# Performance work log

Measured on AMD Instinct MI355X. Metric: run time of the kernel, lower is better.

The kernel has to match this reference:

```python
import jax, jax.numpy as jnp
import numpy as np

N = 100_000          # nodes
E = 3_200_000        # edges (avg degree 32)
DIMS = [6, 20, 15, 10, 5, 2]


def setup_inputs() -> dict:
    key = jax.random.key(0)
    ks = jax.random.split(key, 3 + 2 * 5)
    inp = {
        "x": jax.random.normal(ks[0], (N, DIMS[0]), jnp.float32),
        "edge_index": jax.random.randint(ks[1], (2, E), 0, N, jnp.int32),
        "edge_weight": jax.random.uniform(ks[2], (E,), jnp.float32),
    }
    for i in range(5):
        din, dout = DIMS[i], DIMS[i + 1]
        s = 1.0 / np.sqrt(din)
        inp[f"w_rel{i}"] = jax.random.normal(ks[3 + 2 * i], (din, dout), jnp.float32) * s
        inp[f"b_rel{i}"] = jnp.zeros((dout,), jnp.float32)
        inp[f"w_root{i}"] = jax.random.normal(ks[4 + 2 * i], (din, dout), jnp.float32) * s
    return inp


def _graph_conv(x, src, dst, w, W_rel, b_rel, W_root):
    # PyG GraphConv: lin_rel(scatter_add(w_e * x_src)) + lin_root(x)
    msg = x[src] * w[:, None]                                  # [E, din]
    agg = jax.ops.segment_sum(msg, dst, num_segments=N)        # [N, din]
    return agg @ W_rel + b_rel + x @ W_root                    # [N, dout]


def reference(x, edge_index, edge_weight,
              w_rel0, b_rel0, w_root0,
              w_rel1, b_rel1, w_root1,
              w_rel2, b_rel2, w_root2,
              w_rel3, b_rel3, w_root3,
              w_rel4, b_rel4, w_root4):
    src, dst = edge_index[0], edge_index[1]
    layers = [
        (w_rel0, b_rel0, w_root0),
        (w_rel1, b_rel1, w_root1),
        (w_rel2, b_rel2, w_root2),
        (w_rel3, b_rel3, w_root3),
        (w_rel4, b_rel4, w_root4),
    ]
    for W_rel, b_rel, W_root in layers:
        x = jax.nn.relu(_graph_conv(x, src, dst, edge_weight, W_rel, b_rel, W_root))
    return jax.nn.softmax(x, axis=1)
```

## Files before the change

### kernel.cpp

```cpp
#include <hip/hip_runtime.h>
#include <hip/hip_fp16.h>
#include <stdint.h>

#define N_NODES 100000
#define N_EDGES 3200000
#define BN      128
#define NB      782
#define NCH_H   1024
#define CH_H    (N_EDGES / NCH_H)
#define CPL     (NCH_H / 64)
#define PAD_PER 98
#define NCH_S   512
#define CH_S    (N_EDGES / NCH_S)
#define FPS     (NCH_H / NCH_S)
#define BS1     1024
#define S1_IT   ((CH_S + BS1 - 1) / BS1)
#define BS2     512
#define S2_CAP  4608
#define R2IT    9
#define BLOCK   256
#define W_SCALE 32767.0f
#define W_INV   (1.0f / 32767.0f)

__global__ void hist_kernel(const int* __restrict__ dst, int* __restrict__ hist_g,
                            const float* __restrict__ x, __half* __restrict__ xpad) {
    __shared__ int h[NB];
    for (int b = threadIdx.x; b < NB; b += BLOCK) h[b] = 0;
    {
        int i = blockIdx.x * PAD_PER + threadIdx.x;
        if (threadIdx.x < PAD_PER && i < N_NODES) {
            const float* xr = x + (size_t)i * 6;
            __half2 hh[4];
            hh[0] = __halves2half2(__float2half(xr[0]), __float2half(xr[1]));
            hh[1] = __halves2half2(__float2half(xr[2]), __float2half(xr[3]));
            hh[2] = __halves2half2(__float2half(xr[4]), __float2half(xr[5]));
            hh[3] = __halves2half2(__float2half(0.f),   __float2half(0.f));
            *(uint4*)(xpad + (size_t)i * 8) = *(uint4*)hh;
        }
    }
    __syncthreads();
    const int c  = blockIdx.x;
    const int k0 = c * CH_H;
    for (int k = threadIdx.x; k < CH_H; k += BLOCK)
        atomicAdd(&h[dst[k0 + k] >> 7], 1);
    __syncthreads();
    for (int b = threadIdx.x; b < NB; b += BLOCK)
        hist_g[c * NB + b] = h[b];
}

__global__ void chunkscan_kernel(const int* __restrict__ hist_g,
                                 int* __restrict__ off_g, int* __restrict__ tot) {
    int w    = (blockIdx.x * blockDim.x + threadIdx.x) >> 6;
    int lane = threadIdx.x & 63;
    if (w >= NB) return;
    int v[CPL];
    int ls = 0;
    const int cbase = lane * CPL;
    #pragma unroll
    for (int i = 0; i < CPL; ++i) { v[i] = hist_g[(cbase + i) * NB + w]; ls += v[i]; }
    int run = ls;
    #pragma unroll
    for (int d = 1; d < 64; d <<= 1) {
        int u = __shfl_up(run, d);
        if (lane >= d) run += u;
    }
    int acc = run - ls;
    #pragma unroll
    for (int i = 0; i < CPL; ++i) { off_g[(cbase + i) * NB + w] = acc; acc += v[i]; }
    if (lane == 63) tot[w] = acc;
}

#define SCAN_T   1024
__global__ void scan_kernel(const int* __restrict__ cnt, int* __restrict__ bstart) {
    __shared__ int part[SCAN_T];
    int t = threadIdx.x;
    int v = (t < NB) ? cnt[t] : 0;
    part[t] = v;
    __syncthreads();
    for (int off = 1; off < SCAN_T; off <<= 1) {
        int u = (t >= off) ? part[t - off] : 0;
        __syncthreads();
        part[t] += u;
        __syncthreads();
    }
    if (t < NB) bstart[t] = part[t] - v;
}

__global__ void __launch_bounds__(BS1)
scatter1_kernel(const int* __restrict__ src, const int* __restrict__ dst,
                const float* __restrict__ w,
                const int* __restrict__ bstart, const int* __restrict__ off_g,
                const int* __restrict__ hist_g,
                uint2* __restrict__ rec1) {
    __shared__ uint2 stage[CH_S];
    __shared__ int h[NB];
    __shared__ int delta[NB];
    __shared__ int wtot[BS1 / 64];

    const int c  = blockIdx.x;
    const int k0 = c * CH_S;
    const int t  = threadIdx.x;

    int      dv[S1_IT];
    uint32_t sv[S1_IT];
    float    wv[S1_IT];
    #pragma unroll
    for (int i = 0; i < S1_IT; ++i) {
        int k = t + i * BS1;
        if (k < CH_S) {
            dv[i] = dst[k0 + k];
            sv[i] = (uint32_t)src[k0 + k];
            wv[i] = w[k0 + k];
        }
    }

    for (int b = t; b < NB; b += BS1) {
        int s = 0;
        #pragma unroll
        for (int f = 0; f < FPS; ++f)
            s += hist_g[(size_t)(FPS * c + f) * NB + b];
        h[b] = s;
    }
    __syncthreads();

    {
        const int base = t * 2;
        int v[2], ls = 0;
        #pragma unroll
        for (int i = 0; i < 2; ++i) {
            int idx = base + i;
            v[i] = (idx < NB) ? h[idx] : 0;
            ls += v[i];
        }
        int lane = t & 63, wvi = t >> 6;
        int run = ls;
        #pragma unroll
        for (int d = 1; d < 64; d <<= 1) {
            int u = __shfl_up(run, d);
            if (lane >= d) run += u;
        }
        if (lane == 63) wtot[wvi] = run;
        __syncthreads();
        int wexcl = 0;
        for (int i = 0; i < wvi; ++i) wexcl += wtot[i];
        int excl = wexcl + run - ls;
        #pragma unroll
        for (int i = 0; i < 2; ++i) {
            int idx = base + i;
            if (idx < NB) {
                int gb = bstart[idx] + off_g[(size_t)(FPS * c) * NB + idx];
                h[idx]     = excl;
                delta[idx] = gb - excl;
                excl += v[i];
            }
        }
    }
    __syncthreads();

    #pragma unroll
    for (int i = 0; i < S1_IT; ++i) {
        int k = t + i * BS1;
        if (k < CH_S) {
            int d = dv[i];
            int b = d >> 7;
            int pos = atomicAdd(&h[b], 1);
            uint32_t w15 = (uint32_t)__float2uint_rn(wv[i] * W_SCALE);
            uint2 r;
            r.x = sv[i] | ((uint32_t)(d & 127) << 17);
            r.y = w15 | ((uint32_t)b << 15);
            stage[pos] = r;
        }
    }
    __syncthreads();

    #pragma unroll
    for (int i = 0; i < S1_IT; ++i) {
        int k = t + i * BS1;
        if (k < CH_S) {
            uint2 r = stage[k];
            int b = (int)(r.y >> 15);
            rec1[delta[b] + k] = r;
        }
    }
}

__global__ void __launch_bounds__(BS2)
scatter2_kernel(const uint2* __restrict__ rec1,
                const int* __restrict__ bstart, const int* __restrict__ tot,
                uint32_t* __restrict__ rec2,
                int2* __restrict__ rowcnt) {
    __shared__ int h[BN];
    __shared__ int cur[BN];
    __shared__ int wtot2[2];
    __shared__ uint32_t stage[S2_CAP];
    const int b  = blockIdx.x;
    const int s0 = bstart[b];
    const int n  = tot[b];
    const int t  = threadIdx.x;
    if (t < BN) h[t] = 0;
    __syncthreads();

    uint2 rv[R2IT];
    #pragma unroll
    for (int i = 0; i < R2IT; ++i) {
        int k = t + i * BS2;
        uint2 r = (k < n) ? rec1[s0 + k] : make_uint2(0u, 0u);
        rv[i] = r;
        if (k < n) atomicAdd(&h[r.x >> 17], 1);
    }
    for (int k = t + R2IT * BS2; k < n; k += BS2)
        atomicAdd(&h[rec1[s0 + k].x >> 17], 1);
    __syncthreads();

    int v = 0, run = 0;
    if (t < BN) {
        v = h[t];
        run = v;
        int lane = t & 63;
        #pragma unroll
        for (int d = 1; d < 64; d <<= 1) {
            int u = __shfl_up(run, d);
            if (t >= d && lane >= d) run += u;
        }
        if (lane == 63) wtot2[t >> 6] = run;
    }
    __syncthreads();
    if (t < BN) {
        int excl = run - v + ((t >= 64) ? wtot2[0] : 0);
        cur[t] = excl;
        int node = b * BN + t;
        if (node < N_NODES) rowcnt[node] = make_int2(s0 + excl, v);
    }
    __syncthreads();

    #pragma unroll
    for (int i = 0; i < R2IT; ++i) {
        int k = t + i * BS2;
        if (k < n) {
            uint2 r = rv[i];
            int dl = (int)(r.x >> 17);
            uint32_t r2 = (r.x & 0x1FFFF) | ((r.y & 0x7FFF) << 17);
            int pos = atomicAdd(&cur[dl], 1);
            if (pos < S2_CAP) stage[pos] = r2;
            else              rec2[s0 + pos] = r2;
        }
    }
    for (int k = t + R2IT * BS2; k < n; k += BS2) {
        uint2 r = rec1[s0 + k];
        int dl = (int)(r.x >> 17);
        uint32_t r2 = (r.x & 0x1FFFF) | ((r.y & 0x7FFF) << 17);
        int pos = atomicAdd(&cur[dl], 1);
        if (pos < S2_CAP) stage[pos] = r2;
        else              rec2[s0 + pos] = r2;
    }
    __syncthreads();
    for (int i = t; i < n && i < S2_CAP; i += BS2)
        rec2[s0 + i] = stage[i];
}

__global__ void layer0_kernel(const __half* __restrict__ xpad,
                              const uint32_t* __restrict__ rec,
                              const int2* __restrict__ rowcnt,
                              const float* __restrict__ wrel0, const float* __restrict__ brel0,
                              const float* __restrict__ wroot0,
                              const float* __restrict__ wrel1, const float* __restrict__ brel1,
                              const float* __restrict__ wroot1,
                              __half* __restrict__ pn, float* __restrict__ oinitn) {
    __shared__ float s_wrel0[6 * 20], s_wroot0[6 * 20], s_b0[20];
    __shared__ float s_wrel1[20 * 15], s_wroot1[20 * 15], s_b1[15];
    for (int t = threadIdx.x; t < 120; t += BLOCK) {
        s_wrel0[t]  = wrel0[t];
        s_wroot0[t] = wroot0[t];
    }
    for (int t = threadIdx.x; t < 300; t += BLOCK) {
        s_wrel1[t]  = wrel1[t];
        s_wroot1[t] = wroot1[t];
    }
    if (threadIdx.x < 20) s_b0[threadIdx.x] = brel0[threadIdx.x];
    if (threadIdx.x < 15) s_b1[threadIdx.x] = brel1[threadIdx.x];
    __syncthreads();

    int t = blockIdx.x * blockDim.x + threadIdx.x;
    int node = t >> 3;
    int q    = t & 7;

    float agg[6] = {0.f, 0.f, 0.f, 0.f, 0.f, 0.f};
    const int2 rc = rowcnt[node];
    const int s = rc.x;
    const int e = rc.x + rc.y;
    for (int k = s + q; k < e; k += 32) {
        uint32_t rv[4];
        float    wv[4];
        #pragma unroll
        for (int u = 0; u < 4; ++u) {
            int kk = k + 8 * u;
            int kc = kk < e ? kk : (e - 1);
            rv[u] = rec[kc];
            wv[u] = kk < e ? (float)(rv[u] >> 17) * W_INV : 0.f;
        }
        uint4 raw[4];
        #pragma unroll
        for (int u = 0; u < 4; ++u)
            raw[u] = *(const uint4*)(xpad + (size_t)(rv[u] & 0x1FFFF) * 8);
        #pragma unroll
        for (int u = 0; u < 4; ++u) {
            const __half2* h = (const __half2*)&raw[u];
            float w = wv[u];
            agg[0] += w * __low2float(h[0]);  agg[1] += w * __high2float(h[0]);
            agg[2] += w * __low2float(h[1]);  agg[3] += w * __high2float(h[1]);
            agg[4] += w * __low2float(h[2]);  agg[5] += w * __high2float(h[2]);
        }
    }
    #pragma unroll
    for (int i = 0; i < 6; ++i) {
        agg[i] += __shfl_xor(agg[i], 1);
        agg[i] += __shfl_xor(agg[i], 2);
        agg[i] += __shfl_xor(agg[i], 4);
    }
    uint4 raws = *(const uint4*)(xpad + (size_t)node * 8);
    const __half2* hs = (const __half2*)&raws;
    float xv[6] = { __low2float(hs[0]), __high2float(hs[0]),
                    __low2float(hs[1]), __high2float(hs[1]),
                    __low2float(hs[2]), __high2float(hs[2]) };
    float ov[20];
    #pragma unroll
    for (int j = 0; j < 20; ++j) {
        float o = s_b0[j];
        #pragma unroll
        for (int i = 0; i < 6; ++i)
            o += agg[i] * s_wrel0[i * 20 + j] + xv[i] * s_wroot0[i * 20 + j];
        ov[j] = fmaxf(o, 0.f);
    }
    {
        float pk[2] = {0.f, 0.f};
        #pragma unroll
        for (int kk = 0; kk < 2; ++kk) {
            int k = 2 * q + kk;
            if (k < 15) {
                float sacc = 0.f;
                #pragma unroll
                for (int j = 0; j < 20; ++j) sacc += ov[j] * s_wrel1[j * 15 + k];
                pk[kk] = sacc;
            }
        }
        ((__half2*)(pn + (size_t)node * 16))[q] =
            __halves2half2(__float2half(pk[0]), __float2half(pk[1]));
    }
    #pragma unroll
    for (int kk = 0; kk < 2; ++kk) {
        int k = q + kk * 8;
        if (k < 15) {
            float sacc = s_b1[k];
            #pragma unroll
            for (int j = 0; j < 20; ++j) sacc += ov[j] * s_wroot1[j * 15 + k];
            oinitn[(size_t)node * 15 + k] = sacc;
        }
    }
}

template<int DOUT, int SPH, int NDOUT, int NSPH, bool LAST>
__global__ void gather_kernel(const __half* __restrict__ p, const float* __restrict__ oinit,
                              const uint32_t* __restrict__ rec,
                              const int2* __restrict__ rowcnt,
                              const float* __restrict__ wrel_n, const float* __restrict__ brel_n,
                              const float* __restrict__ wroot_n,
                              __half* __restrict__ pn, float* __restrict__ oinitn,
                              float* __restrict__ out) {
    __shared__ float s_wrel[LAST ? 1 : DOUT * NDOUT];
    __shared__ float s_wroot[LAST ? 1 : DOUT * NDOUT];
    __shared__ float s_b[LAST ? 1 : (NDOUT > 0 ? NDOUT : 1)];
    if constexpr (!LAST) {
        for (int t = threadIdx.x; t < DOUT * NDOUT; t += BLOCK) {
            s_wrel[t]  = wrel_n[t];
            s_wroot[t] = wroot_n[t];
        }
        if (threadIdx.x < NDOUT) s_b[threadIdx.x] = brel_n[threadIdx.x];
        __syncthreads();
    }

    int t = blockIdx.x * blockDim.x + threadIdx.x;
    int node = t >> 3;
    int q    = t & 7;

    float af[SPH];
    #pragma unroll
    for (int i = 0; i < SPH; ++i) af[i] = 0.f;

    const int2 rc = rowcnt[node];
    const int s = rc.x;
    const int e = rc.x + rc.y;
    constexpr int NR = (SPH >= 8) ? SPH / 8 : 1;
    for (int k = s + q; k < e; k += 32) {
        uint32_t rv[4];
        float    wv[4];
        #pragma unroll
        for (int u = 0; u < 4; ++u) {
            int kk = k + 8 * u;
            int kc = kk < e ? kk : (e - 1);
            rv[u] = rec[kc];
            wv[u] = kk < e ? (float)(rv[u] >> 17) * W_INV : 0.f;
        }
        if constexpr (SPH >= 8) {
            uint4 raw[4 * NR];
            #pragma unroll
            for (int u = 0; u < 4; ++u) {
                const uint4* ps = (const uint4*)(p + (size_t)(rv[u] & 0x1FFFF) * SPH);
                #pragma unroll
                for (int v = 0; v < NR; ++v) raw[u * NR + v] = ps[v];
            }
            #pragma unroll
            for (int u = 0; u < 4; ++u) {
                float w = wv[u];
                #pragma unroll
                for (int v = 0; v < NR; ++v) {
                    const __half2* h = (const __half2*)&raw[u * NR + v];
                    #pragma unroll
                    for (int jj = 0; jj < 4; ++jj) {
                        af[v * 8 + 2 * jj]     += w * __low2float(h[jj]);
                        af[v * 8 + 2 * jj + 1] += w * __high2float(h[jj]);
                    }
                }
            }
        } else {
            uint32_t raw[4];
            #pragma unroll
            for (int u = 0; u < 4; ++u)
                raw[u] = *(const uint32_t*)(p + (size_t)(rv[u] & 0x1FFFF) * SPH);
            #pragma unroll
            for (int u = 0; u < 4; ++u) {
                __half2 h = *(const __half2*)&raw[u];
                af[0] += wv[u] * __low2float(h);
                af[1] += wv[u] * __high2float(h);
            }
        }
    }
    #pragma unroll
    for (int i = 0; i < SPH; ++i) {
        af[i] += __shfl_xor(af[i], 1);
        af[i] += __shfl_xor(af[i], 2);
        af[i] += __shfl_xor(af[i], 4);
    }

    if constexpr (LAST) {
        if (q == 0) {
            float o0 = af[0] + oinit[(size_t)node * 2 + 0];
            float o1 = af[1] + oinit[(size_t)node * 2 + 1];
            float m = fmaxf(o0, o1);
            float e0 = __expf(o0 - m), e1 = __expf(o1 - m);
            float inv = 1.f / (e0 + e1);
            out[(size_t)node * 2 + 0] = e0 * inv;
            out[(size_t)node * 2 + 1] = e1 * inv;
        }
    } else {
        float ov[DOUT];
        #pragma unroll
        for (int j = 0; j < DOUT; ++j)
            ov[j] = fmaxf(af[j] + oinit[(size_t)node * DOUT + j], 0.f);

        if (q < NSPH / 2) {
            float pk[2] = {0.f, 0.f};
            #pragma unroll
            for (int kk = 0; kk < 2; ++kk) {
                int k = 2 * q + kk;
                if (k < NDOUT) {
                    float sacc = 0.f;
                    #pragma unroll
                    for (int j = 0; j < DOUT; ++j) sacc += ov[j] * s_wrel[j * NDOUT + k];
                    pk[kk] = sacc;
                }
            }
            ((__half2*)(pn + (size_t)node * NSPH))[q] =
                __halves2half2(__float2half(pk[0]), __float2half(pk[1]));
        }
        #pragma unroll
        for (int kk = 0; kk < 2; ++kk) {
            int k = q + kk * 8;
            if (k < NDOUT) {
                float sacc = s_b[k];
                #pragma unroll
                for (int j = 0; j < DOUT; ++j) sacc += ov[j] * s_wroot[j * NDOUT + k];
                oinitn[(size_t)node * NDOUT + k] = sacc;
            }
        }
    }
}


extern "C" void kernel_launch(void* const* d_in, const int* in_sizes, int n_in,
                              void* d_out, int out_size, void* d_ws, size_t ws_size,
                              hipStream_t stream) {
    const float* x  = (const float*)d_in[0];
    const int*   ei = (const int*)d_in[1];
    const float* ew = (const float*)d_in[2];
    const float* wrel[5]  = { (const float*)d_in[3], (const float*)d_in[6],
                              (const float*)d_in[9], (const float*)d_in[12],
                              (const float*)d_in[15] };
    const float* brel[5]  = { (const float*)d_in[4], (const float*)d_in[7],
                              (const float*)d_in[10], (const float*)d_in[13],
                              (const float*)d_in[16] };
    const float* wroot[5] = { (const float*)d_in[5], (const float*)d_in[8],
                              (const float*)d_in[11], (const float*)d_in[14],
                              (const float*)d_in[17] };

    char* ws = (char*)d_ws;
    size_t off = 0;
    auto alloc = [&](size_t bytes) -> void* {
        void* ptr = ws + off;
        off += (bytes + 255) & ~(size_t)255;
        return ptr;
    };
    char*     regionA   = (char*)alloc((size_t)N_EDGES * 8);
    uint2*    rec1      = (uint2*)regionA;
    __half*   pA        = (__half*)regionA;
    __half*   pB        = (__half*)(regionA + (size_t)4  * 1024 * 1024);
    float*    oA        = (float*)(regionA + (size_t)8  * 1024 * 1024);
    float*    oB        = (float*)(regionA + (size_t)16 * 1024 * 1024);
    uint32_t* rec2      = (uint32_t*)alloc((size_t)N_EDGES * 4);
    __half*   xpad      = (__half*)alloc((size_t)N_NODES * 8 * 2);
    int*      hist_g    = (int*)alloc((size_t)NCH_H * NB * 4);
    int*      off_g     = (int*)alloc((size_t)NCH_H * NB * 4);
    int*      tot       = (int*)alloc((size_t)NB * 4);
    int*      bstart    = (int*)alloc((size_t)NB * 4);
    int2*     rowcnt    = (int2*)alloc((size_t)N_NODES * 8);

    const int* srcv = ei;
    const int* dstv = ei + N_EDGES;

    const int gN8 = (8 * N_NODES + BLOCK - 1) / BLOCK;

    hist_kernel     <<<NCH_H, BLOCK, 0, stream>>>(dstv, hist_g, x, xpad);
    chunkscan_kernel<<<(NB + 3) / 4, BLOCK, 0, stream>>>(hist_g, off_g, tot);
    scan_kernel     <<<1, SCAN_T, 0, stream>>>(tot, bstart);
    scatter1_kernel <<<NCH_S, BS1, 0, stream>>>(srcv, dstv, ew, bstart, off_g, hist_g, rec1);
    scatter2_kernel <<<NB, BS2, 0, stream>>>(rec1, bstart, tot, rec2, rowcnt);

    layer0_kernel<<<gN8, BLOCK, 0, stream>>>(xpad, rec2, rowcnt,
                                             wrel[0], brel[0], wroot[0],
                                             wrel[1], brel[1], wroot[1], pA, oA);
    gather_kernel<15, 16, 10, 16, false><<<gN8, BLOCK, 0, stream>>>(
        pA, oA, rec2, rowcnt, wrel[2], brel[2], wroot[2], pB, oB, nullptr);
    gather_kernel<10, 16, 5, 8, false><<<gN8, BLOCK, 0, stream>>>(
        pB, oB, rec2, rowcnt, wrel[3], brel[3], wroot[3], pA, oA, nullptr);
    gather_kernel<5, 8, 2, 2, false><<<gN8, BLOCK, 0, stream>>>(
        pA, oA, rec2, rowcnt, wrel[4], brel[4], wroot[4], pB, oB, nullptr);
    gather_kernel<2, 2, 0, 0, true><<<gN8, BLOCK, 0, stream>>>(
        pB, oB, rec2, rowcnt, nullptr, nullptr, nullptr,
        nullptr, nullptr, (float*)d_out);
}
```

Measured before the change: 279.6 us.

## Fuse second scatter pass with layer-0 aggregation using shared-memory staged records

Merges the per-bucket scatter kernel with the first graph-conv layer so each block aggregates its 128 destination nodes directly from the shared-memory staged edge records, avoiding a re-read of rec2 from global memory and one kernel launch. Layer buffers are moved out of the aliased rec1 region into separate allocations, since rec1 is still being read while layer-0 outputs are written. The cost is more shared memory and a 512-thread block doing gather work, which may lower occupancy, and fewer, larger blocks for the layer-0 gather than the separate kernel used.

```diff
diff --git a/kernel.cpp b/kernel.cpp
--- a/kernel.cpp
+++ b/kernel.cpp
@@ -185,19 +185,34 @@
 }
 
 __global__ void __launch_bounds__(BS2)
-scatter2_kernel(const uint2* __restrict__ rec1,
-                const int* __restrict__ bstart, const int* __restrict__ tot,
-                uint32_t* __restrict__ rec2,
-                int2* __restrict__ rowcnt) {
+s2l0_kernel(const uint2* __restrict__ rec1,
+            const int* __restrict__ bstart, const int* __restrict__ tot,
+            uint32_t* __restrict__ rec2, int2* __restrict__ rowcnt,
+            const __half* __restrict__ xpad,
+            const float* __restrict__ wrel0, const float* __restrict__ brel0,
+            const float* __restrict__ wroot0,
+            const float* __restrict__ wrel1, const float* __restrict__ brel1,
+            const float* __restrict__ wroot1,
+            __half* __restrict__ pn, float* __restrict__ oinitn) {
     __shared__ int h[BN];
     __shared__ int cur[BN];
+    __shared__ int nstart[BN];
+    __shared__ int ncnt[BN];
     __shared__ int wtot2[2];
     __shared__ uint32_t stage[S2_CAP];
+    __shared__ float s_wrel0[120], s_wroot0[120], s_b0[20];
+    __shared__ float s_wrel1[300], s_wroot1[300], s_b1[15];
+
     const int b  = blockIdx.x;
     const int s0 = bstart[b];
     const int n  = tot[b];
     const int t  = threadIdx.x;
+
     if (t < BN) h[t] = 0;
+    if (t < 120) { s_wrel0[t] = wrel0[t]; s_wroot0[t] = wroot0[t]; }
+    if (t < 300) { s_wrel1[t] = wrel1[t]; s_wroot1[t] = wroot1[t]; }
+    if (t < 20) s_b0[t] = brel0[t];
+    if (t < 15) s_b1[t] = brel1[t];
     __syncthreads();
 
     uint2 rv[R2IT];
@@ -220,7 +235,7 @@
         #pragma unroll
         for (int d = 1; d < 64; d <<= 1) {
             int u = __shfl_up(run, d);
-            if (t >= d && lane >= d) run += u;
+            if (lane >= d) run += u;
         }
         if (lane == 63) wtot2[t >> 6] = run;
     }
@@ -228,6 +243,8 @@
     if (t < BN) {
         int excl = run - v + ((t >= 64) ? wtot2[0] : 0);
         cur[t] = excl;
+        nstart[t] = excl;
+        ncnt[t] = v;
         int node = b * BN + t;
         if (node < N_NODES) rowcnt[node] = make_int2(s0 + excl, v);
     }
@@ -254,106 +271,88 @@
         else              rec2[s0 + pos] = r2;
     }
     __syncthreads();
+
     for (int i = t; i < n && i < S2_CAP; i += BS2)
         rec2[s0 + i] = stage[i];
-}
-
-__global__ void layer0_kernel(const __half* __restrict__ xpad,
-                              const uint32_t* __restrict__ rec,
-                              const int2* __restrict__ rowcnt,
-                              const float* __restrict__ wrel0, const float* __restrict__ brel0,
-                              const float* __restrict__ wroot0,
-                              const float* __restrict__ wrel1, const float* __restrict__ brel1,
-                              const float* __restrict__ wroot1,
-                              __half* __restrict__ pn, float* __restrict__ oinitn) {
-    __shared__ float s_wrel0[6 * 20], s_wroot0[6 * 20], s_b0[20];
-    __shared__ float s_wrel1[20 * 15], s_wroot1[20 * 15], s_b1[15];
-    for (int t = threadIdx.x; t < 120; t += BLOCK) {
-        s_wrel0[t]  = wrel0[t];
-        s_wroot0[t] = wroot0[t];
-    }
-    for (int t = threadIdx.x; t < 300; t += BLOCK) {
-        s_wrel1[t]  = wrel1[t];
-        s_wroot1[t] = wroot1[t];
-    }
-    if (threadIdx.x < 20) s_b0[threadIdx.x] = brel0[threadIdx.x];
-    if (threadIdx.x < 15) s_b1[threadIdx.x] = brel1[threadIdx.x];
-    __syncthreads();
-
-    int t = blockIdx.x * blockDim.x + threadIdx.x;
-    int node = t >> 3;
-    int q    = t & 7;
-
-    float agg[6] = {0.f, 0.f, 0.f, 0.f, 0.f, 0.f};
-    const int2 rc = rowcnt[node];
-    const int s = rc.x;
-    const int e = rc.x + rc.y;
-    for (int k = s + q; k < e; k += 32) {
-        uint32_t rv[4];
-        float    wv[4];
-        #pragma unroll
-        for (int u = 0; u < 4; ++u) {
-            int kk = k + 8 * u;
-            int kc = kk < e ? kk : (e - 1);
-            rv[u] = rec[kc];
-            wv[u] = kk < e ? (float)(rv[u] >> 17) * W_INV : 0.f;
-        }
-        uint4 raw[4];
-        #pragma unroll
-        for (int u = 0; u < 4; ++u)
-            raw[u] = *(const uint4*)(xpad + (size_t)(rv[u] & 0x1FFFF) * 8);
-        #pragma unroll
-        for (int u = 0; u < 4; ++u) {
-            const __half2* h = (const __half2*)&raw[u];
-            float w = wv[u];
-            agg[0] += w * __low2float(h[0]);  agg[1] += w * __high2float(h[0]);
-            agg[2] += w * __low2float(h[1]);  agg[3] += w * __high2float(h[1]);
-            agg[4] += w * __low2float(h[2]);  agg[5] += w * __high2float(h[2]);
-        }
-    }
-    #pragma unroll
-    for (int i = 0; i < 6; ++i) {
-        agg[i] += __shfl_xor(agg[i], 1);
-        agg[i] += __shfl_xor(agg[i], 2);
-        agg[i] += __shfl_xor(agg[i], 4);
-    }
-    uint4 raws = *(const uint4*)(xpad + (size_t)node * 8);
-    const __half2* hs = (const __half2*)&raws;
-    float xv[6] = { __low2float(hs[0]), __high2float(hs[0]),
-                    __low2float(hs[1]), __high2float(hs[1]),
-                    __low2float(hs[2]), __high2float(hs[2]) };
-    float ov[20];
-    #pragma unroll
-    for (int j = 0; j < 20; ++j) {
-        float o = s_b0[j];
-        #pragma unroll
-        for (int i = 0; i < 6; ++i)
-            o += agg[i] * s_wrel0[i * 20 + j] + xv[i] * s_wroot0[i * 20 + j];
-        ov[j] = fmaxf(o, 0.f);
-    }
-    {
-        float pk[2] = {0.f, 0.f};
-        #pragma unroll
-        for (int kk = 0; kk < 2; ++kk) {
-            int k = 2 * q + kk;
-            if (k < 15) {
-                float sacc = 0.f;
+
+    #pragma unroll
+    for (int half = 0; half < 2; ++half) {
+        const int dl   = half * 64 + (t >> 3);
+        const int q    = t & 7;
+        const int node = b * BN + dl;
+        const int s = nstart[dl];
+        const int e = s + ncnt[dl];
+        float agg[6] = {0.f, 0.f, 0.f, 0.f, 0.f, 0.f};
+        for (int k = s + q; k < e; k += 32) {
+            uint32_t tok[4];
+            float    wv4[4];
+            #pragma unroll
+            for (int u = 0; u < 4; ++u) {
+                int kk = k + 8 * u;
+                int kc = kk < e ? kk : (e - 1);
+                uint32_t r2 = (kc < S2_CAP) ? stage[kc] : rec2[s0 + kc];
+                tok[u] = r2;
+                wv4[u] = kk < e ? (float)(r2 >> 17) * W_INV : 0.f;
+            }
+            uint4 raw[4];
+            #pragma unroll
+            for (int u = 0; u < 4; ++u)
+                raw[u] = *(const uint4*)(xpad + (size_t)(tok[u] & 0x1FFFF) * 8);
+            #pragma unroll
+            for (int u = 0; u < 4; ++u) {
+                const __half2* hh = (const __half2*)&raw[u];
+                float w = wv4[u];
+                agg[0] += w * __low2float(hh[0]);  agg[1] += w * __high2float(hh[0]);
+                agg[2] += w * __low2float(hh[1]);  agg[3] += w * __high2float(hh[1]);
+                agg[4] += w * __low2float(hh[2]);  agg[5] += w * __high2float(hh[2]);
+            }
+        }
+        #pragma unroll
+        for (int i = 0; i < 6; ++i) {
+            agg[i] += __shfl_xor(agg[i], 1);
+            agg[i] += __shfl_xor(agg[i], 2);
+            agg[i] += __shfl_xor(agg[i], 4);
+        }
+        if (node < N_NODES) {
+            uint4 raws = *(const uint4*)(xpad + (size_t)node * 8);
+            const __half2* hs = (const __half2*)&raws;
+            float xv[6] = { __low2float(hs[0]), __high2float(hs[0]),
+                            __low2float(hs[1]), __high2float(hs[1]),
+                            __low2float(hs[2]), __high2float(hs[2]) };
+            float ov[20];
+            #pragma unroll
+            for (int j = 0; j < 20; ++j) {
+                float o = s_b0[j];
                 #pragma unroll
-                for (int j = 0; j < 20; ++j) sacc += ov[j] * s_wrel1[j * 15 + k];
-                pk[kk] = sacc;
-            }
-        }
-        ((__half2*)(pn + (size_t)node * 16))[q] =
-            __halves2half2(__float2half(pk[0]), __float2half(pk[1]));
-    }
-    #pragma unroll
-    for (int kk = 0; kk < 2; ++kk) {
-        int k = q + kk * 8;
-        if (k < 15) {
-            float sacc = s_b1[k];
-            #pragma unroll
-            for (int j = 0; j < 20; ++j) sacc += ov[j] * s_wroot1[j * 15 + k];
-            oinitn[(size_t)node * 15 + k] = sacc;
+                for (int i = 0; i < 6; ++i)
+                    o += agg[i] * s_wrel0[i * 20 + j] + xv[i] * s_wroot0[i * 20 + j];
+                ov[j] = fmaxf(o, 0.f);
+            }
+            {
+                float pk[2] = {0.f, 0.f};
+                #pragma unroll
+                for (int kk = 0; kk < 2; ++kk) {
+                    int k = 2 * q + kk;
+                    if (k < 15) {
+                        float sacc = 0.f;
+                        #pragma unroll
+                        for (int j = 0; j < 20; ++j) sacc += ov[j] * s_wrel1[j * 15 + k];
+                        pk[kk] = sacc;
+                    }
+                }
+                ((__half2*)(pn + (size_t)node * 16))[q] =
+                    __halves2half2(__float2half(pk[0]), __float2half(pk[1]));
+            }
+            #pragma unroll
+            for (int kk = 0; kk < 2; ++kk) {
+                int k = q + kk * 8;
+                if (k < 15) {
+                    float sacc = s_b1[k];
+                    #pragma unroll
+                    for (int j = 0; j < 20; ++j) sacc += ov[j] * s_wroot1[j * 15 + k];
+                    oinitn[(size_t)node * 15 + k] = sacc;
+                }
+            }
         }
     }
 }
@@ -509,13 +508,12 @@
         off += (bytes + 255) & ~(size_t)255;
         return ptr;
     };
-    char*     regionA   = (char*)alloc((size_t)N_EDGES * 8);
-    uint2*    rec1      = (uint2*)regionA;
-    __half*   pA        = (__half*)regionA;
-    __half*   pB        = (__half*)(regionA + (size_t)4  * 1024 * 1024);
-    float*    oA        = (float*)(regionA + (size_t)8  * 1024 * 1024);
-    float*    oB        = (float*)(regionA + (size_t)16 * 1024 * 1024);
+    uint2*    rec1      = (uint2*)alloc((size_t)N_EDGES * 8);
     uint32_t* rec2      = (uint32_t*)alloc((size_t)N_EDGES * 4);
+    __half*   pA        = (__half*)alloc((size_t)N_NODES * 16 * 2);
+    __half*   pB        = (__half*)alloc((size_t)N_NODES * 16 * 2);
+    float*    oA        = (float*)alloc((size_t)N_NODES * 15 * 4);
+    float*    oB        = (float*)alloc((size_t)N_NODES * 15 * 4);
     __half*   xpad      = (__half*)alloc((size_t)N_NODES * 8 * 2);
     int*      hist_g    = (int*)alloc((size_t)NCH_H * NB * 4);
     int*      off_g     = (int*)alloc((size_t)NCH_H * NB * 4);
@@ -532,11 +530,11 @@
     chunkscan_kernel<<<(NB + 3) / 4, BLOCK, 0, stream>>>(hist_g, off_g, tot);
     scan_kernel     <<<1, SCAN_T, 0, stream>>>(tot, bstart);
     scatter1_kernel <<<NCH_S, BS1, 0, stream>>>(srcv, dstv, ew, bstart, off_g, hist_g, rec1);
-    scatter2_kernel <<<NB, BS2, 0, stream>>>(rec1, bstart, tot, rec2, rowcnt);
-
-    layer0_kernel<<<gN8, BLOCK, 0, stream>>>(xpad, rec2, rowcnt,
-                                             wrel[0], brel[0], wroot[0],
-                                             wrel[1], brel[1], wroot[1], pA, oA);
+
+    s2l0_kernel<<<NB, BS2, 0, stream>>>(rec1, bstart, tot, rec2, rowcnt, xpad,
+                                        wrel[0], brel[0], wroot[0],
+                                        wrel[1], brel[1], wroot[1], pA, oA);
+
     gather_kernel<15, 16, 10, 16, false><<<gN8, BLOCK, 0, stream>>>(
         pA, oA, rec2, rowcnt, wrel[2], brel[2], wroot[2], pB, oB, nullptr);
     gather_kernel<10, 16, 5, 8, false><<<gN8, BLOCK, 0, stream>>>(
```

After: 310.9 us. +11.2%, slower.

## Replace per-chunk offset scan with global atomic bucket cursors in scatter

Applied to the files above, without the earlier changes.

Swaps the chunk-by-bucket exclusive scan (which wrote a large off_g table) for a plain per-bucket reduction. Each scatter1 block now claims its bucket ranges with an atomicAdd on a global cursor seeded by the bucket-start scan. This removes the off_g writes and reads, though the order of edges within a bucket becomes nondeterministic. It also simplifies tail handling in the gather loops and drops a redundant condition in the scatter2 scan.

```diff
diff --git a/kernel.cpp b/kernel.cpp
--- a/kernel.cpp
+++ b/kernel.cpp
@@ -48,30 +48,22 @@
         hist_g[c * NB + b] = h[b];
 }
 
-__global__ void chunkscan_kernel(const int* __restrict__ hist_g,
-                                 int* __restrict__ off_g, int* __restrict__ tot) {
+__global__ void reduce_kernel(const int* __restrict__ hist_g, int* __restrict__ tot) {
     int w    = (blockIdx.x * blockDim.x + threadIdx.x) >> 6;
     int lane = threadIdx.x & 63;
     if (w >= NB) return;
-    int v[CPL];
     int ls = 0;
     const int cbase = lane * CPL;
     #pragma unroll
-    for (int i = 0; i < CPL; ++i) { v[i] = hist_g[(cbase + i) * NB + w]; ls += v[i]; }
-    int run = ls;
-    #pragma unroll
-    for (int d = 1; d < 64; d <<= 1) {
-        int u = __shfl_up(run, d);
-        if (lane >= d) run += u;
-    }
-    int acc = run - ls;
-    #pragma unroll
-    for (int i = 0; i < CPL; ++i) { off_g[(cbase + i) * NB + w] = acc; acc += v[i]; }
-    if (lane == 63) tot[w] = acc;
+    for (int i = 0; i < CPL; ++i) ls += hist_g[(cbase + i) * NB + w];
+    #pragma unroll
+    for (int d = 32; d >= 1; d >>= 1) ls += __shfl_xor(ls, d);
+    if (lane == 0) tot[w] = ls;
 }
 
 #define SCAN_T   1024
-__global__ void scan_kernel(const int* __restrict__ cnt, int* __restrict__ bstart) {
+__global__ void scan_kernel(const int* __restrict__ cnt, int* __restrict__ bstart,
+                            int* __restrict__ gcur) {
     __shared__ int part[SCAN_T];
     int t = threadIdx.x;
     int v = (t < NB) ? cnt[t] : 0;
@@ -83,13 +75,13 @@
         part[t] += u;
         __syncthreads();
     }
-    if (t < NB) bstart[t] = part[t] - v;
+    if (t < NB) { int e = part[t] - v; bstart[t] = e; gcur[t] = e; }
 }
 
 __global__ void __launch_bounds__(BS1)
 scatter1_kernel(const int* __restrict__ src, const int* __restrict__ dst,
                 const float* __restrict__ w,
-                const int* __restrict__ bstart, const int* __restrict__ off_g,
+                int* __restrict__ gcur,
                 const int* __restrict__ hist_g,
                 uint2* __restrict__ rec1) {
     __shared__ uint2 stage[CH_S];
@@ -148,7 +140,7 @@
         for (int i = 0; i < 2; ++i) {
             int idx = base + i;
             if (idx < NB) {
-                int gb = bstart[idx] + off_g[(size_t)(FPS * c) * NB + idx];
+                int gb = atomicAdd(&gcur[idx], v[i]);
                 h[idx]     = excl;
                 delta[idx] = gb - excl;
                 excl += v[i];
@@ -220,7 +212,7 @@
         #pragma unroll
         for (int d = 1; d < 64; d <<= 1) {
             int u = __shfl_up(run, d);
-            if (t >= d && lane >= d) run += u;
+            if (lane >= d) run += u;
         }
         if (lane == 63) wtot2[t >> 6] = run;
     }
@@ -294,9 +286,8 @@
         #pragma unroll
         for (int u = 0; u < 4; ++u) {
             int kk = k + 8 * u;
-            int kc = kk < e ? kk : (e - 1);
-            rv[u] = rec[kc];
-            wv[u] = kk < e ? (float)(rv[u] >> 17) * W_INV : 0.f;
+            rv[u] = (kk < e) ? rec[kk] : 0u;
+            wv[u] = (float)(rv[u] >> 17) * W_INV;
         }
         uint4 raw[4];
         #pragma unroll
@@ -396,9 +387,8 @@
         #pragma unroll
         for (int u = 0; u < 4; ++u) {
             int kk = k + 8 * u;
-            int kc = kk < e ? kk : (e - 1);
-            rv[u] = rec[kc];
-            wv[u] = kk < e ? (float)(rv[u] >> 17) * W_INV : 0.f;
+            rv[u] = (kk < e) ? rec[kk] : 0u;
+            wv[u] = (float)(rv[u] >> 17) * W_INV;
         }
         if constexpr (SPH >= 8) {
             uint4 raw[4 * NR];
@@ -518,9 +508,9 @@
     uint32_t* rec2      = (uint32_t*)alloc((size_t)N_EDGES * 4);
     __half*   xpad      = (__half*)alloc((size_t)N_NODES * 8 * 2);
     int*      hist_g    = (int*)alloc((size_t)NCH_H * NB * 4);
-    int*      off_g     = (int*)alloc((size_t)NCH_H * NB * 4);
     int*      tot       = (int*)alloc((size_t)NB * 4);
     int*      bstart    = (int*)alloc((size_t)NB * 4);
+    int*      gcur      = (int*)alloc((size_t)NB * 4);
     int2*     rowcnt    = (int2*)alloc((size_t)N_NODES * 8);
 
     const int* srcv = ei;
@@ -528,11 +518,11 @@
 
     const int gN8 = (8 * N_NODES + BLOCK - 1) / BLOCK;
 
-    hist_kernel     <<<NCH_H, BLOCK, 0, stream>>>(dstv, hist_g, x, xpad);
-    chunkscan_kernel<<<(NB + 3) / 4, BLOCK, 0, stream>>>(hist_g, off_g, tot);
-    scan_kernel     <<<1, SCAN_T, 0, stream>>>(tot, bstart);
-    scatter1_kernel <<<NCH_S, BS1, 0, stream>>>(srcv, dstv, ew, bstart, off_g, hist_g, rec1);
-    scatter2_kernel <<<NB, BS2, 0, stream>>>(rec1, bstart, tot, rec2, rowcnt);
+    hist_kernel    <<<NCH_H, BLOCK, 0, stream>>>(dstv, hist_g, x, xpad);
+    reduce_kernel  <<<(NB + 3) / 4, BLOCK, 0, stream>>>(hist_g, tot);
+    scan_kernel    <<<1, SCAN_T, 0, stream>>>(tot, bstart, gcur);
+    scatter1_kernel<<<NCH_S, BS1, 0, stream>>>(srcv, dstv, ew, gcur, hist_g, rec1);
+    scatter2_kernel<<<NB, BS2, 0, stream>>>(rec1, bstart, tot, rec2, rowcnt);
 
     layer0_kernel<<<gN8, BLOCK, 0, stream>>>(xpad, rec2, rowcnt,
                                              wrel[0], brel[0], wroot[0],
```

Measured after the change: 282.3 us. No clear change (+0.9%).
